# Performance work log

Hardware: AMD Instinct MI355X
Metric: run time of the kernel (lower is better)

Reference implementation:

```python
import jax, jax.numpy as jnp
import numpy as np

N_NODES = 100_000
N_EDGES = 1_600_000
IN_FEATS = 64
H_DIMS = 64
OUT_A = 2
OUT_B = 21
N_LAYERS = 2
EPS = 1e-5


def setup_inputs() -> dict:
    key = jax.random.key(0)
    ks = jax.random.split(key, 16)
    d = H_DIMS

    def rn(k, shape, scale=0.05):
        return jax.random.normal(k, shape, dtype=jnp.float32) * scale

    return {
        "v": jax.random.normal(ks[0], (N_NODES, IN_FEATS), dtype=jnp.float32),
        "src": jax.random.randint(ks[1], (N_EDGES,), 0, N_NODES),
        "dst": jax.random.randint(ks[2], (N_EDGES,), 0, N_NODES),
        "rel_type": jax.random.randint(ks[3], (N_EDGES,), 0, 3),
        "norm": jax.random.uniform(ks[4], (N_EDGES,), dtype=jnp.float32),
        "emb_W": rn(ks[5], (d, IN_FEATS)),
        "emb_b": jnp.zeros((d,), jnp.float32),
        "emb_gamma": jnp.ones((d,), jnp.float32),
        "emb_beta": jnp.zeros((d,), jnp.float32),
        "rel_weight": rn(ks[6], (3, d, d)),
        "gru_Wih": rn(ks[7], (3 * d, d)),
        "gru_Whh": rn(ks[8], (3 * d, d)),
        "gru_bih": jnp.zeros((3 * d,), jnp.float32),
        "gru_bhh": jnp.zeros((3 * d,), jnp.float32),
        "ker_gamma": jnp.ones((d,), jnp.float32),
        "ker_beta": jnp.zeros((d,), jnp.float32),
        "a_W1": rn(ks[9], (d, d)), "a_b1": jnp.zeros((d,), jnp.float32),
        "a_gamma": jnp.ones((d,), jnp.float32), "a_beta": jnp.zeros((d,), jnp.float32),
        "a_W2": rn(ks[10], (OUT_A, d)), "a_b2": jnp.zeros((OUT_A,), jnp.float32),
        "b_W1": rn(ks[11], (d, d)), "b_b1": jnp.zeros((d,), jnp.float32),
        "b_gamma": jnp.ones((d,), jnp.float32), "b_beta": jnp.zeros((d,), jnp.float32),
        "b_W2": rn(ks[12], (OUT_B, d)), "b_b2": jnp.zeros((OUT_B,), jnp.float32),
    }


def _bn(x, gamma, beta):
    # BatchNorm1d in training mode: batch statistics, biased variance
    mu = jnp.mean(x, axis=0)
    var = jnp.var(x, axis=0)
    return (x - mu) * jax.lax.rsqrt(var + EPS) * gamma + beta


def _gru_cell(x, h, Wih, Whh, bih, bhh):
    # torch nn.GRU single layer, gate order (r, z, n)
    gi = x @ Wih.T + bih
    gh = h @ Whh.T + bhh
    ir, iz, inn = jnp.split(gi, 3, axis=-1)
    hr, hz, hn = jnp.split(gh, 3, axis=-1)
    r = jax.nn.sigmoid(ir + hr)
    z = jax.nn.sigmoid(iz + hz)
    n = jnp.tanh(inn + r * hn)
    return (1.0 - z) * n + z * h


def reference(v, src, dst, rel_type, norm, emb_W, emb_b, emb_gamma, emb_beta,
              rel_weight, gru_Wih, gru_Whh, gru_bih, gru_bhh, ker_gamma, ker_beta,
              a_W1, a_b1, a_gamma, a_beta, a_W2, a_b2,
              b_W1, b_b1, b_gamma, b_beta, b_W2, b_b2):
    # Embedding: Linear -> BN -> ReLU
    h0 = jax.nn.relu(_bn(v @ emb_W.T + emb_b, emb_gamma, emb_beta))
    output = h0
    h = jnp.zeros_like(h0)
    n_nodes = v.shape[0]
    for _ in range(N_LAYERS):
        # per-node relational transform for all 3 relations: [N, 3, d]
        x3 = jnp.einsum('nd,rdk->nrk', output, rel_weight)
        msg = x3[src, rel_type] * norm[:, None]                     # [E, d]
        swh = jax.ops.segment_sum(msg, dst, num_segments=n_nodes)   # [N, d]
        h = _gru_cell(swh, h, gru_Wih, gru_Whh, gru_bih, gru_bhh)
        output = h
    hk = _bn(output, ker_gamma, ker_beta)
    # task heads: Linear -> BN -> ReLU -> Linear (MLP with h_layers=2)
    xa = jax.nn.relu(_bn(hk @ a_W1.T + a_b1, a_gamma, a_beta)) @ a_W2.T + a_b2
    xb = jax.nn.relu(_bn(hk @ b_W1.T + b_b1, b_gamma, b_beta)) @ b_W2.T + b_b2
    return xa, xb
```

## Files before the change

kernel.cpp:

```cpp
#include <hip/hip_runtime.h>

#define NN 100000
#define NE 1600000
#define NP 100096
#define NBKT 391
#define CAP 6144
#define EPSV 1e-5f

typedef unsigned int u32;
typedef unsigned short u16;
typedef unsigned long long u64;
typedef __bf16 bf16x8 __attribute__((ext_vector_type(8)));
typedef float f32x4 __attribute__((ext_vector_type(4)));

#define GLBP(x) ((const __attribute__((address_space(1))) u32*)(x))
#define LDSP(x) ((__attribute__((address_space(3))) u32*)(x))

__device__ __forceinline__ u16 f2bf(float f) {
  u32 x = __float_as_uint(f);
  return (u16)((x + 0x7FFFu + ((x >> 16) & 1u)) >> 16);
}
__device__ __forceinline__ float bf2f(u16 h) { return __uint_as_float(((u32)h) << 16); }

__device__ __forceinline__ void pack_one(const float* W, u32* out, int K, int KOT, int i) {
  int q = i & 3, lane = (i >> 2) & 63, f = i >> 8;
  int ks = f / KOT, ot = f - ks * KOT;
  int o = ot * 16 + (lane & 15);
  int k = ks * 32 + (lane >> 4) * 8 + q * 2;
  out[i] = (u32)f2bf(W[o * K + k]) | ((u32)f2bf(W[o * K + k + 1]) << 16);
}

__global__ void setupA(const float* __restrict__ relw, const float* __restrict__ Wih,
                       const float* __restrict__ embW, const float* __restrict__ Whh,
                       float* __restrict__ Wrow, u32* __restrict__ PWem, u32* __restrict__ PWhh) {
  int b = blockIdx.x;
  if (b < 144) {
    int t = b * 256 + threadIdx.x;
    if (t >= 192 * 192) return;
    int kg = t / 192, j = t % 192;
    const float* a = relw + (j >> 6) * 4096 + (j & 63) * 64;
    const float* w = Wih + kg * 64;
    float s = 0.f;
#pragma unroll
    for (int k = 0; k < 64; ++k) s += a[k] * w[k];
    Wrow[kg * 192 + j] = s;
  } else if (b < 152) {
    pack_one(embW, PWem, 64, 4, (b - 144) * 256 + threadIdx.x);
  } else {
    pack_one(Whh, PWhh, 64, 12, (b - 152) * 256 + threadIdx.x);
  }
}

__global__ void pack_wf(const float* __restrict__ Wrow, u32* __restrict__ PWf) {
  pack_one(Wrow, PWf, 192, 12, blockIdx.x * 256 + threadIdx.x);
}

__global__ void fold_pack(const float* __restrict__ Wa, const float* __restrict__ Wb,
                          const float* __restrict__ kacc, const float* __restrict__ kg,
                          u32* __restrict__ P) {
  int i = blockIdx.x * 256 + threadIdx.x;
  int q = i & 3, lane = (i >> 2) & 63, f = i >> 8;
  int ks = f >> 3, ot = f & 7;
  int o = ot * 16 + (lane & 15);
  int k = ks * 32 + (lane >> 4) * 8 + q * 2;
  const float* W = (o < 64) ? (Wa + o * 64) : (Wb + (o - 64) * 64);
  const float inv = 1.f / NN;
  float m0 = kacc[k] * inv;
  float s0 = kg[k] * rsqrtf(kacc[64 + k] * inv - m0 * m0 + EPSV);
  float m1 = kacc[k + 1] * inv;
  float s1 = kg[k + 1] * rsqrtf(kacc[64 + k + 1] * inv - m1 * m1 + EPSV);
  P[i] = (u32)f2bf(W[k] * s0) | ((u32)f2bf(W[k + 1] * s1) << 16);
}

__global__ __launch_bounds__(256) void countplace(const int* __restrict__ src,
                                                  const int* __restrict__ dst,
                                                  const int* __restrict__ rt,
                                                  const float* __restrict__ nrm,
                                                  int* __restrict__ gcnt,
                                                  u64* __restrict__ region) {
  __shared__ u32 hist[NBKT], gbase[NBKT];
  const int t = threadIdx.x;
  for (int i = t; i < NBKT; i += 256) hist[i] = 0;
  __syncthreads();
  const int e0 = blockIdx.x * 2048 + t;
  u32 rlo[8], rhi[8], lrank[8];
  int bkt[8];
#pragma unroll
  for (int i = 0; i < 8; ++i) {
    int e = e0 + i * 256;
    bkt[i] = -1;
    if (e < NE) {
      int d = dst[e];
      int b = d >> 8;
      bkt[i] = b;
      lrank[i] = atomicAdd(&hist[b], 1u);
      rlo[i] = (u32)src[e] | ((u32)rt[e] << 20) | ((u32)(d & 255) << 22);
      rhi[i] = __float_as_uint(nrm[e]);
    }
  }
  __syncthreads();
  for (int i = t; i < NBKT; i += 256) {
    u32 h = hist[i];
    gbase[i] = h ? (u32)atomicAdd(&gcnt[i], (int)h) : 0u;
  }
  __syncthreads();
#pragma unroll
  for (int i = 0; i < 8; ++i) {
    if (bkt[i] >= 0) {
      u32 pos = gbase[bkt[i]] + lrank[i];
      if (pos < CAP)
        region[(size_t)bkt[i] * CAP + pos] = (u64)rlo[i] | ((u64)rhi[i] << 32);
    }
  }
}

__global__ __launch_bounds__(512) void bucketscan(const int* __restrict__ gcnt,
                                                  int* __restrict__ bbase) {
  int t = threadIdx.x;
  int v = (t < NBKT) ? gcnt[t] : 0;
  __shared__ int sh[512];
  sh[t] = v;
  __syncthreads();
#pragma unroll
  for (int off = 1; off < 512; off <<= 1) {
    int u = (t >= off) ? sh[t - off] : 0;
    __syncthreads();
    sh[t] += u;
    __syncthreads();
  }
  if (t < NBKT) bbase[t] = sh[t] - v;
}

__global__ __launch_bounds__(256) void localsort(const int* __restrict__ gcnt,
                                                 const int* __restrict__ bbase,
                                                 const u64* __restrict__ region,
                                                 u64* __restrict__ csr,
                                                 int* __restrict__ rowpr) {
  const int b = blockIdx.x, t = threadIdx.x;
  int n = gcnt[b];
  if (n > CAP) n = CAP;
  const int base = bbase[b];
  __shared__ u32 hist[1024], sc[256];
#pragma unroll
  for (int i = 0; i < 4; ++i) hist[t + 256 * i] = 0;
  __syncthreads();
  for (int i = t; i < n; i += 256)
    atomicAdd(&hist[(u32)(region[(size_t)b * CAP + i] >> 20) & 1023u], 1u);
  __syncthreads();
  u32 a0 = hist[4 * t], a1 = hist[4 * t + 1], a2 = hist[4 * t + 2], a3 = hist[4 * t + 3];
  u32 part = a0 + a1 + a2 + a3;
  sc[t] = part;
  __syncthreads();
#pragma unroll
  for (int off = 1; off < 256; off <<= 1) {
    u32 u = (t >= off) ? sc[t - off] : 0;
    __syncthreads();
    sc[t] += u;
    __syncthreads();
  }
  u32 ex = sc[t] - part;
  int node = b * 256 + t;
  rowpr[4 * node + 0] = base + (int)ex;
  rowpr[4 * node + 1] = base + (int)(ex + a0);
  rowpr[4 * node + 2] = base + (int)(ex + a0 + a1);
  rowpr[4 * node + 3] = base + (int)(ex + a0 + a1 + a2);
  __syncthreads();
  hist[4 * t] = ex; hist[4 * t + 1] = ex + a0;
  hist[4 * t + 2] = ex + a0 + a1; hist[4 * t + 3] = ex + a0 + a1 + a2;
  __syncthreads();
  for (int i = t; i < n; i += 256) {
    u64 rec = region[(size_t)b * CAP + i];
    u32 pos = atomicAdd(&hist[(u32)(rec >> 20) & 1023u], 1u);
    csr[(size_t)base + pos] = rec;
  }
}

__global__ __launch_bounds__(256) void csr_gather(const int* __restrict__ rowpr,
                                                  const u64* __restrict__ csr,
                                                  const u16* __restrict__ Xbf,
                                                  u16* __restrict__ ACCbf) {
  int wv = blockIdx.x * 4 + (threadIdx.x >> 6);
  int lane = threadIdx.x & 63;
  if (wv >= NN) return;
  const int half = lane >> 5, c2 = lane & 31;
  int4 rp = *reinterpret_cast<const int4*>(rowpr + 4 * wv);
  const int bnd[4] = {rp.x, rp.y, rp.z, rp.w};
  u32* orow = (u32*)(ACCbf + (size_t)wv * 192);
#define PAIRF(J)                                                                  \
  { u32 sA = (u32)__builtin_amdgcn_readlane((int)lo, (J));                        \
    u32 sB = (u32)__builtin_amdgcn_readlane((int)lo, (J) + 1);                    \
    u32 nA = (u32)__builtin_amdgcn_readlane((int)hi, (J));                        \
    u32 nB = (u32)__builtin_amdgcn_readlane((int)hi, (J) + 1);                    \
    u32 srp = half ? sB : sA;                                                     \
    float nm = __uint_as_float(half ? nB : nA);                                   \
    u32 xw = *(const u32*)(Xbf + (size_t)(srp & 0xFFFFFu) * 64 + 2 * c2);         \
    ax = fmaf(__uint_as_float(xw << 16), nm, ax);                                 \
    ay = fmaf(__uint_as_float(xw & 0xFFFF0000u), nm, ay); }
#pragma unroll
  for (int r = 0; r < 3; ++r) {
    int b0 = bnd[r], e0 = bnd[r + 1];
    float ax = 0.f, ay = 0.f;
    for (int c = b0; c < e0; c += 64) {
      int m = e0 - c; m = m > 64 ? 64 : m;
      u32 lo = 0, hi = 0;
      if (lane < m) {
        u64 rec = csr[(size_t)c + lane];
        lo = (u32)rec; hi = (u32)(rec >> 32);
      }
      int j = 0;
      for (; j + 4 <= m; j += 4) { PAIRF(j) PAIRF(j + 2) }
      for (; j + 2 <= m; j += 2) { PAIRF(j) }
      if (j < m) {
        u32 sA = (u32)__builtin_amdgcn_readlane((int)lo, j);
        u32 nA = (u32)__builtin_amdgcn_readlane((int)hi, j);
        float nm = __uint_as_float(half ? 0u : nA);
        u32 xw = *(const u32*)(Xbf + (size_t)(sA & 0xFFFFFu) * 64 + 2 * c2);
        ax = fmaf(__uint_as_float(xw << 16), nm, ax);
        ay = fmaf(__uint_as_float(xw & 0xFFFF0000u), nm, ay);
      }
    }
    ax += __shfl_xor(ax, 32);
    ay += __shfl_xor(ay, 32);
    if (half == 0) orow[r * 32 + c2] = (u32)f2bf(ax) | ((u32)f2bf(ay) << 16);
  }
#undef PAIRF
}

template<int K, int KO, int AF32, int GRU, int CS, int OUTBF>
__global__ __launch_bounds__(256) void gemm_mfma(
    const void* __restrict__ Av, const u32* __restrict__ Wpk, void* __restrict__ Yv,
    const float* __restrict__ bih, const float* __restrict__ bhh,
    const u16* __restrict__ G2B, const u16* __restrict__ Hv,
    float* __restrict__ csum, int n) {
  constexpr int KOT = KO / 16, KS = K / 32;
  constexpr int NFRAG = KS * KOT;
  __shared__ u32 bsh[NFRAG * 256];
  __shared__ float cs[2 * KO];
  const int lane = threadIdx.x & 63, w = threadIdx.x >> 6;
  const int rr = lane & 15, kg = lane >> 4;
  const long mbase = (long)blockIdx.x * 128 + w * 32;
  const u16* Abf = (const u16*)Av;
  const float* Af = (const float*)Av;

  auto loadAbf = [&](int ks, int halfsel) -> bf16x8 {
    if (AF32) {
      long r = mbase + halfsel * 16 + rr;
      if (r > n - 1) r = n - 1;
      const float* pp = Af + r * K + ks * 32 + kg * 8;
      float4 u0 = *(const float4*)pp;
      float4 u1 = *(const float4*)(pp + 4);
      bf16x8 o_;
      o_[0] = __builtin_bit_cast(__bf16, f2bf(u0.x));
      o_[1] = __builtin_bit_cast(__bf16, f2bf(u0.y));
      o_[2] = __builtin_bit_cast(__bf16, f2bf(u0.z));
      o_[3] = __builtin_bit_cast(__bf16, f2bf(u0.w));
      o_[4] = __builtin_bit_cast(__bf16, f2bf(u1.x));
      o_[5] = __builtin_bit_cast(__bf16, f2bf(u1.y));
      o_[6] = __builtin_bit_cast(__bf16, f2bf(u1.z));
      o_[7] = __builtin_bit_cast(__bf16, f2bf(u1.w));
      return o_;
    }
    return *reinterpret_cast<const bf16x8*>(Abf + (mbase + halfsel * 16 + rr) * K + ks * 32 + kg * 8);
  };

  constexpr int PASSES = NFRAG / 4;
#pragma unroll
  for (int i = 0; i < PASSES; ++i) {
    int c = i * 4 + w;
    __builtin_amdgcn_global_load_lds(GLBP(Wpk + (long)c * 256 + lane * 4),
                                     LDSP(&bsh[c * 256]), 16, 0, 0);
  }
  bf16x8 a0 = loadAbf(0, 0);
  bf16x8 a1 = loadAbf(0, 1);
  __syncthreads();

  f32x4 acc[2][KOT] = {};
#pragma unroll
  for (int ks = 0; ks < KS; ++ks) {
    bf16x8 c0 = a0, c1 = a1;
    if (ks + 1 < KS) {
      a0 = loadAbf(ks + 1, 0);
      a1 = loadAbf(ks + 1, 1);
    }
#pragma unroll
    for (int o = 0; o < KOT; ++o) {
      bf16x8 bfr = *reinterpret_cast<const bf16x8*>(&bsh[((ks * KOT + o) * 64 + lane) * 4]);
      acc[0][o] = __builtin_amdgcn_mfma_f32_16x16x32_bf16(c0, bfr, acc[0][o], 0, 0, 0);
      acc[1][o] = __builtin_amdgcn_mfma_f32_16x16x32_bf16(c1, bfr, acc[1][o], 0, 0, 0);
    }
  }

  float s[KOT] = {}, ss[KOT] = {};
  if (GRU == 0) {
#pragma unroll
    for (int tl = 0; tl < 2; ++tl)
#pragma unroll
      for (int o = 0; o < KOT; ++o)
#pragma unroll
        for (int q = 0; q < 4; ++q) {
          long row = mbase + tl * 16 + kg * 4 + q;
          float vv = acc[tl][o][q];
          if (row < n) {
            long off = row * KO + o * 16 + rr;
            if (OUTBF) ((u16*)Yv)[off] = f2bf(vv);
            else       ((float*)Yv)[off] = vv;
            if (CS) { s[o] += vv; ss[o] += vv * vv; }
          }
        }
  } else {
    float bi[12], bh_[12];
#pragma unroll
    for (int g = 0; g < 3; ++g)
#pragma unroll
      for (int o = 0; o < 4; ++o) {
        bi[g * 4 + o] = bih[g * 64 + o * 16 + rr];
        bh_[g * 4 + o] = bhh[g * 64 + o * 16 + rr];
      }
#pragma unroll
    for (int tl = 0; tl < 2; ++tl)
#pragma unroll
      for (int o = 0; o < 4; ++o) {
        int c = o * 16 + rr;
#pragma unroll
        for (int q = 0; q < 4; ++q) {
          long row = mbase + tl * 16 + kg * 4 + q;
          float ir = acc[tl][o][q] + bi[o];
          float iz = acc[tl][o + 4][q] + bi[4 + o];
          float in_ = acc[tl][o + 8][q] + bi[8 + o];
          float hr = bh_[o], hz = bh_[4 + o], hn = bh_[8 + o], hv = 0.f;
          if (GRU == 2) {
            const u16* g2 = G2B + row * 192;
            hr += bf2f(g2[c]); hz += bf2f(g2[64 + c]); hn += bf2f(g2[128 + c]);
            hv = bf2f(Hv[row * 64 + c]);
          }
          float rg = 1.f / (1.f + __expf(-(ir + hr)));
          float zg = 1.f / (1.f + __expf(-(iz + hz)));
          float ng = tanhf(in_ + rg * hn);
          float h = (1.f - zg) * ng + (GRU == 2 ? zg * hv : 0.f);
          if (row < n) {
            ((u16*)Yv)[row * 64 + c] = f2bf(h);
            if (CS) { s[o] += h; ss[o] += h * h; }
          }
        }
      }
  }
  if (CS) {
    constexpr int LIM = (GRU == 0) ? 2 * KO : 128;
    constexpr int CKO = (GRU == 0) ? KO : 64;
    constexpr int OL = (GRU == 0) ? KOT : 4;
    for (int i = threadIdx.x; i < LIM; i += 256) cs[i] = 0.f;
    __syncthreads();
#pragma unroll
    for (int o = 0; o < OL; ++o) {
      int c = o * 16 + rr;
      atomicAdd(&cs[c], s[o]);
      atomicAdd(&cs[CKO + c], ss[o]);
    }
    __syncthreads();
    for (int i = threadIdx.x; i < LIM; i += 256) atomicAdd(&csum[i], cs[i]);
  }
}

__global__ __launch_bounds__(256) void bn_apply_bf(const float* __restrict__ X,
                                                   u16* __restrict__ Y,
                                                   const float* __restrict__ accs,
                                                   const float* __restrict__ gamma,
                                                   const float* __restrict__ beta, int relu) {
  __shared__ float scsh[128];
  int t = threadIdx.x;
  if (t < 64) {
    float mean = accs[t] * (1.f / NN);
    float var = accs[64 + t] * (1.f / NN) - mean * mean;
    float sc = gamma[t] * rsqrtf(var + EPSV);
    scsh[t] = sc;
    scsh[64 + t] = beta[t] - mean * sc;
  }
  __syncthreads();
  long i = (long)blockIdx.x * 256 + t;
  float4 v = reinterpret_cast<const float4*>(X)[i];
  int c = (int)((i * 4) & 63);
  v.x = fmaf(v.x, scsh[c],     scsh[64 + c]);
  v.y = fmaf(v.y, scsh[c + 1], scsh[65 + c]);
  v.z = fmaf(v.z, scsh[c + 2], scsh[66 + c]);
  v.w = fmaf(v.w, scsh[c + 3], scsh[67 + c]);
  if (relu) {
    v.x = fmaxf(v.x, 0.f); v.y = fmaxf(v.y, 0.f);
    v.z = fmaxf(v.z, 0.f); v.w = fmaxf(v.w, 0.f);
  }
  reinterpret_cast<ushort4*>(Y)[i] = make_ushort4(f2bf(v.x), f2bf(v.y), f2bf(v.z), f2bf(v.w));
}

template<int KO>
__global__ __launch_bounds__(256) void headfin_bn(const u16* __restrict__ Z,
                                                  const float* __restrict__ asum,
                                                  const float* __restrict__ asq,
                                                  const float* __restrict__ gamma,
                                                  const float* __restrict__ beta,
                                                  const float* __restrict__ W2,
                                                  const float* __restrict__ b2,
                                                  float* __restrict__ out, int n) {
  __shared__ float ws[KO * 64];
  __shared__ float scsh[128];
  int t = threadIdx.x;
  if (t < 64) {
    float mean = asum[t] * (1.f / NN);
    float var = asq[t] * (1.f / NN) - mean * mean;
    float sc = gamma[t] * rsqrtf(var + EPSV);
    scsh[t] = sc;
    scsh[64 + t] = beta[t] - mean * sc;
  }
  for (int i = t; i < KO * 64; i += 256) ws[i] = W2[i];
  __syncthreads();
  long node = (long)blockIdx.x * 256 + t;
  if (node >= n) return;
  const u16* zr = Z + node * 128;
  float x[64];
#pragma unroll
  for (int i = 0; i < 16; ++i) {
    ushort4 z4 = reinterpret_cast<const ushort4*>(zr)[i];
    int c = i * 4;
    x[c]     = fmaxf(fmaf(bf2f(z4.x), scsh[c],     scsh[64 + c]), 0.f);
    x[c + 1] = fmaxf(fmaf(bf2f(z4.y), scsh[c + 1], scsh[65 + c]), 0.f);
    x[c + 2] = fmaxf(fmaf(bf2f(z4.z), scsh[c + 2], scsh[66 + c]), 0.f);
    x[c + 3] = fmaxf(fmaf(bf2f(z4.w), scsh[c + 3], scsh[67 + c]), 0.f);
  }
#pragma unroll
  for (int o = 0; o < KO; ++o) {
    float a = b2[o];
#pragma unroll
    for (int d = 0; d < 64; ++d) a = fmaf(x[d], ws[o * 64 + d], a);
    out[node * KO + o] = a;
  }
}

extern "C" void kernel_launch(void* const* d_in, const int* in_sizes, int n_in,
                              void* d_out, int out_size, void* d_ws, size_t ws_size,
                              hipStream_t stream) {
  const float* v     = (const float*)d_in[0];
  const int*   src   = (const int*)d_in[1];
  const int*   dst   = (const int*)d_in[2];
  const int*   rt    = (const int*)d_in[3];
  const float* norm  = (const float*)d_in[4];
  const float* emb_W = (const float*)d_in[5];
  const float* emb_g  = (const float*)d_in[7];
  const float* emb_be = (const float*)d_in[8];
  const float* rel_w  = (const float*)d_in[9];
  const float* Wih    = (const float*)d_in[10];
  const float* Whh    = (const float*)d_in[11];
  const float* bih    = (const float*)d_in[12];
  const float* bhh    = (const float*)d_in[13];
  const float* ker_g  = (const float*)d_in[14];
  const float* aW1    = (const float*)d_in[16];
  const float* a_g  = (const float*)d_in[18];
  const float* a_be = (const float*)d_in[19];
  const float* aW2  = (const float*)d_in[20];
  const float* ab2  = (const float*)d_in[21];
  const float* bW1  = (const float*)d_in[22];
  const float* b_g  = (const float*)d_in[24];
  const float* b_be = (const float*)d_in[25];
  const float* bW2  = (const float*)d_in[26];
  const float* bb2  = (const float*)d_in[27];
  float* out = (float*)d_out;

  char* p = (char*)d_ws;
  auto nxt = [&](size_t bytes) -> char* {
    char* r = p; p += (bytes + 255) & ~(size_t)255; return r;
  };
  int*   GCNT = (int*)nxt(512 * 4);
  float* ACCs = (float*)nxt(512 * 4);
  float* Z    = (float*)nxt((size_t)NP * 64 * 4);
  u16*   X1   = (u16*)nxt((size_t)NP * 64 * 2);
  u16*   X2   = (u16*)nxt((size_t)NP * 64 * 2);
  u16*   ACCB = (u16*)nxt((size_t)NP * 192 * 2);
  u16*   G2B  = (u16*)nxt((size_t)NP * 192 * 2);
  u64*   REG  = (u64*)nxt((size_t)NBKT * CAP * 8);
  u64*   CSR  = (u64*)nxt((size_t)NE * 8);
  int*   BBAS = (int*)nxt(512 * 4);
  int*   ROWPR = (int*)nxt((size_t)(NP + 8) * 4 * 4);
  u32*   PWf  = (u32*)nxt(18432 * 4);
  u32*   PWem = (u32*)nxt(2048 * 4);
  u32*   PWhh = (u32*)nxt(6144 * 4);
  u32*   PWab = (u32*)nxt(4096 * 4);
  float* WROW = (float*)nxt(147456);

  hipMemsetAsync(GCNT, 0, 1024 * 4, stream);

  setupA<<<176, 256, 0, stream>>>(rel_w, Wih, emb_W, Whh, WROW, PWem, PWhh);
  countplace<<<782, 256, 0, stream>>>(src, dst, rt, norm, GCNT, REG);
  bucketscan<<<1, 512, 0, stream>>>(GCNT, BBAS);
  localsort<<<NBKT, 256, 0, stream>>>(GCNT, BBAS, REG, CSR, ROWPR);
  pack_wf<<<72, 256, 0, stream>>>(WROW, PWf);

  gemm_mfma<64, 64, 1, 0, 1, 0><<<782, 256, 0, stream>>>(v, PWem, Z, nullptr, nullptr,
                                                         nullptr, nullptr, ACCs + 0, NN);
  bn_apply_bf<<<6250, 256, 0, stream>>>(Z, X2, ACCs + 0, emb_g, emb_be, 1);

  csr_gather<<<25000, 256, 0, stream>>>(ROWPR, CSR, X2, ACCB);
  gemm_mfma<192, 192, 0, 1, 0, 1><<<782, 256, 0, stream>>>(ACCB, PWf, X1, bih, bhh,
                                                           nullptr, nullptr, nullptr, NN);

  csr_gather<<<25000, 256, 0, stream>>>(ROWPR, CSR, X1, ACCB);
  gemm_mfma<64, 192, 0, 0, 0, 1><<<782, 256, 0, stream>>>(X1, PWhh, G2B, nullptr, nullptr,
                                                          nullptr, nullptr, nullptr, NN);
  gemm_mfma<192, 192, 0, 2, 1, 1><<<782, 256, 0, stream>>>(ACCB, PWf, X1, bih, bhh,
                                                           G2B, X1, ACCs + 128, NN);

  fold_pack<<<16, 256, 0, stream>>>(aW1, bW1, ACCs + 128, ker_g, PWab);
  gemm_mfma<64, 128, 0, 0, 1, 1><<<782, 256, 0, stream>>>(X1, PWab, ACCB, nullptr, nullptr,
                                                          nullptr, nullptr, ACCs + 256, NN);
  headfin_bn<2><<<391, 256, 0, stream>>>((const u16*)ACCB, ACCs + 256, ACCs + 384,
                                         a_g, a_be, aW2, ab2, out, NN);
  headfin_bn<21><<<391, 256, 0, stream>>>((const u16*)ACCB + 64, ACCs + 320, ACCs + 448,
                                          b_g, b_be, bW2, bb2, out + (long)NN * 2, NN);
}
```

Before: 414.2 us.

## Pad per-relation CSR segments to even length and merge gather loops

Each (node, relation) edge segment in the CSR is padded to an even count, with zero records filling the odd slot, and bucket bases get extra slack to hold the padding. The gather kernel now walks a node's three relation segments in one chunked loop and handles them with pairwise-only inner loops, dropping the odd-tail special case. It also loads each 64-edge chunk once instead of once per relation. The cost is extra CSR memory, extra padded-edge work, and an extra write pass in localsort.

```diff
diff --git a/kernel.cpp b/kernel.cpp
--- a/kernel.cpp
+++ b/kernel.cpp
@@ -117,7 +117,7 @@
 __global__ __launch_bounds__(512) void bucketscan(const int* __restrict__ gcnt,
                                                   int* __restrict__ bbase) {
   int t = threadIdx.x;
-  int v = (t < NBKT) ? gcnt[t] : 0;
+  int v = (t < NBKT) ? (gcnt[t] + 768) : 0;
   __shared__ int sh[512];
   sh[t] = v;
   __syncthreads();
@@ -147,8 +147,9 @@
   for (int i = t; i < n; i += 256)
     atomicAdd(&hist[(u32)(region[(size_t)b * CAP + i] >> 20) & 1023u], 1u);
   __syncthreads();
-  u32 a0 = hist[4 * t], a1 = hist[4 * t + 1], a2 = hist[4 * t + 2], a3 = hist[4 * t + 3];
-  u32 part = a0 + a1 + a2 + a3;
+  u32 a0 = hist[4 * t], a1 = hist[4 * t + 1], a2 = hist[4 * t + 2];
+  u32 p0 = (a0 + 1) & ~1u, p1 = (a1 + 1) & ~1u, p2 = (a2 + 1) & ~1u;
+  u32 part = p0 + p1 + p2;
   sc[t] = part;
   __syncthreads();
 #pragma unroll
@@ -161,18 +162,23 @@
   u32 ex = sc[t] - part;
   int node = b * 256 + t;
   rowpr[4 * node + 0] = base + (int)ex;
-  rowpr[4 * node + 1] = base + (int)(ex + a0);
-  rowpr[4 * node + 2] = base + (int)(ex + a0 + a1);
-  rowpr[4 * node + 3] = base + (int)(ex + a0 + a1 + a2);
-  __syncthreads();
-  hist[4 * t] = ex; hist[4 * t + 1] = ex + a0;
-  hist[4 * t + 2] = ex + a0 + a1; hist[4 * t + 3] = ex + a0 + a1 + a2;
+  rowpr[4 * node + 1] = base + (int)(ex + p0);
+  rowpr[4 * node + 2] = base + (int)(ex + p0 + p1);
+  rowpr[4 * node + 3] = base + (int)(ex + p0 + p1 + p2);
+  __syncthreads();
+  hist[4 * t + 0] = ex;
+  hist[4 * t + 1] = ex + p0;
+  hist[4 * t + 2] = ex + p0 + p1;
   __syncthreads();
   for (int i = t; i < n; i += 256) {
     u64 rec = region[(size_t)b * CAP + i];
     u32 pos = atomicAdd(&hist[(u32)(rec >> 20) & 1023u], 1u);
     csr[(size_t)base + pos] = rec;
   }
+  __syncthreads();
+  if (a0 & 1) csr[(size_t)base + ex + a0] = 0ull;
+  if (a1 & 1) csr[(size_t)base + ex + p0 + a1] = 0ull;
+  if (a2 & 1) csr[(size_t)base + ex + p0 + p1 + a2] = 0ull;
 }
 
 __global__ __launch_bounds__(256) void csr_gather(const int* __restrict__ rowpr,
@@ -184,46 +190,49 @@
   if (wv >= NN) return;
   const int half = lane >> 5, c2 = lane & 31;
   int4 rp = *reinterpret_cast<const int4*>(rowpr + 4 * wv);
-  const int bnd[4] = {rp.x, rp.y, rp.z, rp.w};
-  u32* orow = (u32*)(ACCbf + (size_t)wv * 192);
-#define PAIRF(J)                                                                  \
-  { u32 sA = (u32)__builtin_amdgcn_readlane((int)lo, (J));                        \
-    u32 sB = (u32)__builtin_amdgcn_readlane((int)lo, (J) + 1);                    \
-    u32 nA = (u32)__builtin_amdgcn_readlane((int)hi, (J));                        \
-    u32 nB = (u32)__builtin_amdgcn_readlane((int)hi, (J) + 1);                    \
-    u32 srp = half ? sB : sA;                                                     \
-    float nm = __uint_as_float(half ? nB : nA);                                   \
-    u32 xw = *(const u32*)(Xbf + (size_t)(srp & 0xFFFFFu) * 64 + 2 * c2);         \
-    ax = fmaf(__uint_as_float(xw << 16), nm, ax);                                 \
-    ay = fmaf(__uint_as_float(xw & 0xFFFF0000u), nm, ay); }
-#pragma unroll
-  for (int r = 0; r < 3; ++r) {
-    int b0 = bnd[r], e0 = bnd[r + 1];
-    float ax = 0.f, ay = 0.f;
-    for (int c = b0; c < e0; c += 64) {
-      int m = e0 - c; m = m > 64 ? 64 : m;
-      u32 lo = 0, hi = 0;
-      if (lane < m) {
-        u64 rec = csr[(size_t)c + lane];
-        lo = (u32)rec; hi = (u32)(rec >> 32);
-      }
-      int j = 0;
-      for (; j + 4 <= m; j += 4) { PAIRF(j) PAIRF(j + 2) }
-      for (; j + 2 <= m; j += 2) { PAIRF(j) }
-      if (j < m) {
-        u32 sA = (u32)__builtin_amdgcn_readlane((int)lo, j);
-        u32 nA = (u32)__builtin_amdgcn_readlane((int)hi, j);
-        float nm = __uint_as_float(half ? 0u : nA);
-        u32 xw = *(const u32*)(Xbf + (size_t)(sA & 0xFFFFFu) * 64 + 2 * c2);
-        ax = fmaf(__uint_as_float(xw << 16), nm, ax);
-        ay = fmaf(__uint_as_float(xw & 0xFFFF0000u), nm, ay);
-      }
-    }
-    ax += __shfl_xor(ax, 32);
-    ay += __shfl_xor(ay, 32);
-    if (half == 0) orow[r * 32 + c2] = (u32)f2bf(ax) | ((u32)f2bf(ay) << 16);
-  }
-#undef PAIRF
+  const int b0 = __builtin_amdgcn_readfirstlane(rp.x);
+  const int b1 = __builtin_amdgcn_readfirstlane(rp.y);
+  const int b2 = __builtin_amdgcn_readfirstlane(rp.z);
+  const int b3 = __builtin_amdgcn_readfirstlane(rp.w);
+  const u32* X4 = (const u32*)Xbf;
+  float a0x = 0.f, a0y = 0.f, a1x = 0.f, a1y = 0.f, a2x = 0.f, a2y = 0.f;
+#define PAIRB(J, AX, AY)                                                        \
+  { u32 sA = (u32)__builtin_amdgcn_readlane((int)lo, (J));                      \
+    u32 sB = (u32)__builtin_amdgcn_readlane((int)lo, (J) + 1);                  \
+    u32 nA = (u32)__builtin_amdgcn_readlane((int)hi, (J));                      \
+    u32 nB = (u32)__builtin_amdgcn_readlane((int)hi, (J) + 1);                  \
+    u32 srp = half ? sB : sA;                                                   \
+    float nm = __uint_as_float(half ? nB : nA);                                 \
+    u32 xw = X4[((srp & 0xFFFFFu) << 5) | (u32)c2];                             \
+    AX = fmaf(__uint_as_float(xw << 16), nm, AX);                               \
+    AY = fmaf(__uint_as_float(xw & 0xFFFF0000u), nm, AY); }
+  for (int c = b0; c < b3; c += 64) {
+    int m = b3 - c; m = m > 64 ? 64 : m;
+    u32 lo = 0, hi = 0;
+    if (lane < m) {
+      u64 rec = csr[(size_t)c + lane];
+      lo = (u32)rec; hi = (u32)(rec >> 32);
+    }
+    int j1 = b1 - c; j1 = j1 < 0 ? 0 : (j1 > m ? m : j1);
+    int j2 = b2 - c; j2 = j2 < 0 ? 0 : (j2 > m ? m : j2);
+    int j = 0;
+    for (; j + 4 <= j1; j += 4) { PAIRB(j, a0x, a0y) PAIRB(j + 2, a0x, a0y) }
+    if (j < j1) { PAIRB(j, a0x, a0y) j += 2; }
+    for (; j + 4 <= j2; j += 4) { PAIRB(j, a1x, a1y) PAIRB(j + 2, a1x, a1y) }
+    if (j < j2) { PAIRB(j, a1x, a1y) j += 2; }
+    for (; j + 4 <= m; j += 4) { PAIRB(j, a2x, a2y) PAIRB(j + 2, a2x, a2y) }
+    if (j < m) { PAIRB(j, a2x, a2y) j += 2; }
+  }
+#undef PAIRB
+  a0x += __shfl_xor(a0x, 32); a0y += __shfl_xor(a0y, 32);
+  a1x += __shfl_xor(a1x, 32); a1y += __shfl_xor(a1y, 32);
+  a2x += __shfl_xor(a2x, 32); a2y += __shfl_xor(a2y, 32);
+  if (half == 0) {
+    u32* orow = (u32*)(ACCbf + (size_t)wv * 192);
+    orow[c2]      = (u32)f2bf(a0x) | ((u32)f2bf(a0y) << 16);
+    orow[32 + c2] = (u32)f2bf(a1x) | ((u32)f2bf(a1y) << 16);
+    orow[64 + c2] = (u32)f2bf(a2x) | ((u32)f2bf(a2y) << 16);
+  }
 }
 
 template<int K, int KO, int AF32, int GRU, int CS, int OUTBF>
@@ -474,7 +483,7 @@
   u16*   ACCB = (u16*)nxt((size_t)NP * 192 * 2);
   u16*   G2B  = (u16*)nxt((size_t)NP * 192 * 2);
   u64*   REG  = (u64*)nxt((size_t)NBKT * CAP * 8);
-  u64*   CSR  = (u64*)nxt((size_t)NE * 8);
+  u64*   CSR  = (u64*)nxt((size_t)(NE + NBKT * 768 + 64) * 8);
   int*   BBAS = (int*)nxt(512 * 4);
   int*   ROWPR = (int*)nxt((size_t)(NP + 8) * 4 * 4);
   u32*   PWf  = (u32*)nxt(18432 * 4);
```

Result: faster. 380.7 us (-8.1%).
